# Optimization experiments

Measured on AMD Instinct MI355X. Metric: run time of the kernel, lower is better.

Reference implementation:

```python
import jax, jax.numpy as jnp
import numpy as np

N_NODES = 50000
N_EDGES = 800000
IN_DIM, HID_DIM, OUT_DIM = 128, 128, 64


def setup_inputs() -> dict:
    key = jax.random.key(0)
    ks = jax.random.split(key, 8)
    x = jax.random.normal(ks[0], (N_NODES, IN_DIM), dtype=jnp.float32)
    edge_index = jax.random.randint(ks[1], (2, N_EDGES), 0, N_NODES, dtype=jnp.int64)
    # GCNConv uses Glorot weights + zero bias; any random init is fine for a reference
    W1 = jax.random.normal(ks[2], (IN_DIM, HID_DIM), dtype=jnp.float32) / np.sqrt(IN_DIM)
    b1 = jnp.zeros((HID_DIM,), dtype=jnp.float32)
    W2 = jax.random.normal(ks[3], (HID_DIM, OUT_DIM), dtype=jnp.float32) / np.sqrt(HID_DIM)
    b2 = jnp.zeros((OUT_DIM,), dtype=jnp.float32)
    Wfc = jax.random.normal(ks[4], (OUT_DIM, 2), dtype=jnp.float32) / np.sqrt(OUT_DIM)
    bfc = jnp.zeros((2,), dtype=jnp.float32)
    return {"x": x, "edge_index": edge_index, "W1": W1, "b1": b1,
            "W2": W2, "b2": b2, "Wfc": Wfc, "bfc": bfc}


def _gcn_conv(x, src, dst, W, b, n_nodes):
    """PyG GCNConv: out = D^{-1/2} (A+I) D^{-1/2} (x W) + b."""
    xw = x @ W  # [N, F_out] transform before propagation
    ones = jnp.ones(src.shape[0], dtype=xw.dtype)
    deg = jax.ops.segment_sum(ones, dst, num_segments=n_nodes) + 1.0  # +1 for self-loop
    dinv = jax.lax.rsqrt(deg)
    norm = dinv[src] * dinv[dst]  # [E]
    msg = xw[src] * norm[:, None]  # gather + scale: [E, F_out]
    agg = jax.ops.segment_sum(msg, dst, num_segments=n_nodes)  # scatter-add
    agg = agg + xw * (dinv * dinv)[:, None]  # self-loop contribution (norm = 1/deg)
    return agg + b


def reference(x, edge_index, W1, b1, W2, b2, Wfc, bfc):
    n = x.shape[0]
    src, dst = edge_index[0], edge_index[1]
    h = jax.nn.relu(_gcn_conv(x, src, dst, W1, b1, n))
    # dropout is identity in eval mode
    h = _gcn_conv(h, src, dst, W2, b2, n)
    h = h @ Wfc + bfc
    return jax.nn.leaky_relu(h, negative_slope=0.01)
```

## Files before the change

### kernel.cpp

```cpp
#include <hip/hip_runtime.h>
#include <hip/hip_fp16.h>

#define IN_DIM 128
#define HID_DIM 128
#define OUT_DIM 64
#define BINW 128
#define BINSHIFT 7
#define MAXBIN 512
#define CAP 4096
#define CNTSTRIDE 16

__global__ __launch_bounds__(256) void k_scatter(const int* __restrict__ src,
                                                 const int* __restrict__ dst,
                                                 int* __restrict__ bin_cnt,
                                                 int* __restrict__ ovf_cnt,
                                                 unsigned int* __restrict__ ovf,
                                                 unsigned int* __restrict__ ebin,
                                                 int E, int nbin) {
    __shared__ int h[MAXBIN];
    __shared__ int base_s[MAXBIN];
    int t = threadIdx.x;
    for (int k = t; k < nbin; k += 256) h[k] = 0;
    __syncthreads();
    int per = E / gridDim.x;
    int ebeg = blockIdx.x * per;
    int eend = (blockIdx.x + 1 == gridDim.x) ? E : ebeg + per;
    for (int i = ebeg + t; i < eend; i += 256)
        atomicAdd(&h[dst[i] >> BINSHIFT], 1);
    __syncthreads();
    for (int k = t; k < nbin; k += 256) {
        int c = h[k];
        base_s[k] = (c > 0) ? atomicAdd(&bin_cnt[k * CNTSTRIDE], c) : 0;
        h[k] = 0;
    }
    __syncthreads();
    for (int i = ebeg + t; i < eend; i += 256) {
        unsigned int s = (unsigned int)src[i];
        unsigned int d = (unsigned int)dst[i];
        int b = (int)(d >> BINSHIFT);
        int pos = base_s[b] + atomicAdd(&h[b], 1);
        unsigned int packed = s | (d << 16);
        if (pos < CAP) ebin[(size_t)b * CAP + pos] = packed;
        else ovf[atomicAdd(ovf_cnt, 1)] = packed;
    }
}

__global__ __launch_bounds__(256) void k_fill(const unsigned int* __restrict__ ebin,
                                              const int* __restrict__ bin_cnt,
                                              const int* __restrict__ ovf_cnt,
                                              const unsigned int* __restrict__ ovf,
                                              int* __restrict__ row_ptr,
                                              unsigned short* __restrict__ degu,
                                              unsigned short* __restrict__ csr_src,
                                              float* __restrict__ dinv,
                                              const float* __restrict__ W2,
                                              const float* __restrict__ Wfc,
                                              const float* __restrict__ b2,
                                              const float* __restrict__ bfc,
                                              float* __restrict__ Wc,
                                              float* __restrict__ bc,
                                              int N, int nbin) {
    __shared__ int cnt[BINW];
    __shared__ int excl[BINW];
    __shared__ int start[BINW];
    int k = blockIdx.x;
    int node0 = k * BINW;
    int nn = min(BINW, N - node0);
    int t = threadIdx.x;
    if (t < BINW) cnt[t] = 0;
    __syncthreads();
    int cnt_k = min(bin_cnt[k * CNTSTRIDE], CAP);
    const unsigned int* seg = ebin + (size_t)k * CAP;
    for (int i = t; i < cnt_k; i += 256)
        atomicAdd(&cnt[(seg[i] >> 16) & (BINW - 1)], 1);
    int novf = *ovf_cnt;
    for (int i = t; i < novf; i += 256) {
        unsigned int e = ovf[i];
        if ((int)(e >> (16 + BINSHIFT)) == k)
            atomicAdd(&cnt[(e >> 16) & (BINW - 1)], 1);
    }
    __syncthreads();
    if (t < BINW) excl[t] = (t < nn) ? cnt[t] : 0;
    __syncthreads();
    for (int off = 1; off < BINW; off <<= 1) {
        int u = 0;
        if (t < BINW && t >= off) u = excl[t - off];
        __syncthreads();
        if (t < BINW) excl[t] += u;
        __syncthreads();
    }
    if (t < nn) {
        int deg = cnt[t];
        int e0 = k * CAP + excl[t] - deg;
        start[t] = e0;
        row_ptr[node0 + t] = e0;
        degu[node0 + t] = (unsigned short)deg;
        dinv[node0 + t] = rsqrtf((float)deg + 1.0f);
        cnt[t] = 0;
    }
    __syncthreads();
    for (int i = t; i < cnt_k; i += 256) {
        unsigned int e = seg[i];
        int dl = (e >> 16) & (BINW - 1);
        int slot = start[dl] + atomicAdd(&cnt[dl], 1);
        csr_src[slot] = (unsigned short)(e & 0xffffu);
    }
    for (int i = t; i < novf; i += 256) {
        unsigned int e = ovf[i];
        if ((int)(e >> (16 + BINSHIFT)) == k) {
            int dl = (e >> 16) & (BINW - 1);
            int slot = start[dl] + atomicAdd(&cnt[dl], 1);
            csr_src[slot] = (unsigned short)(e & 0xffffu);
        }
    }
    if (k == 0) {
        int kk = t >> 1, j = t & 1;
        float acc = 0.f;
#pragma unroll 8
        for (int m = 0; m < OUT_DIM; ++m) acc += W2[kk * OUT_DIM + m] * Wfc[m * 2 + j];
        Wc[kk * 2 + j] = acc;
        if (kk == 0) {
            float b = 0.f;
#pragma unroll 8
            for (int m = 0; m < OUT_DIM; ++m) b += b2[m] * Wfc[m * 2 + j];
            bc[j] = b + bfc[j];
        }
    }
}

__global__ __launch_bounds__(256) void k_gemm1(const float* __restrict__ x,
                                               const float* __restrict__ W,
                                               const float* __restrict__ dinv,
                                               __half* __restrict__ xwh, int N) {
    __shared__ float Ws[64][128];
    int tid = threadIdx.x;
    float4* Ws4 = (float4*)&Ws[0][0];
    int tx = tid & 15, ty = tid >> 4;
    int row0 = blockIdx.x * 128;
    int rows[8];
    const float* xr[8];
#pragma unroll
    for (int j = 0; j < 8; ++j) {
        int row = row0 + ty + 16 * j;
        rows[j] = row;
        if (row > N - 1) row = N - 1;
        xr[j] = x + (size_t)row * IN_DIM;
    }
    float4 aclo[8], achi[8];
#pragma unroll
    for (int j = 0; j < 8; ++j) {
        aclo[j] = make_float4(0.f, 0.f, 0.f, 0.f);
        achi[j] = make_float4(0.f, 0.f, 0.f, 0.f);
    }
#pragma unroll
    for (int ph = 0; ph < 2; ++ph) {
        const float4* W4 = (const float4*)(W + (size_t)ph * 64 * HID_DIM);
#pragma unroll
        for (int i = 0; i < 8; ++i) Ws4[tid + 256 * i] = W4[tid + 256 * i];
        __syncthreads();
#pragma unroll 2
        for (int k4 = 0; k4 < 16; ++k4) {
            float4 av[8];
#pragma unroll
            for (int j = 0; j < 8; ++j) av[j] = *(const float4*)(xr[j] + ph * 64 + k4 * 4);
#pragma unroll
            for (int kk = 0; kk < 4; ++kk) {
                float4 blo = *(const float4*)&Ws[k4 * 4 + kk][4 * tx];
                float4 bhi = *(const float4*)&Ws[k4 * 4 + kk][64 + 4 * tx];
#pragma unroll
                for (int j = 0; j < 8; ++j) {
                    float a = (kk == 0) ? av[j].x : (kk == 1) ? av[j].y : (kk == 2) ? av[j].z : av[j].w;
                    aclo[j].x += a * blo.x; aclo[j].y += a * blo.y;
                    aclo[j].z += a * blo.z; aclo[j].w += a * blo.w;
                    achi[j].x += a * bhi.x; achi[j].y += a * bhi.y;
                    achi[j].z += a * bhi.z; achi[j].w += a * bhi.w;
                }
            }
        }
        __syncthreads();
    }
#pragma unroll
    for (int j = 0; j < 8; ++j) {
        if (rows[j] < N) {
            float dd = dinv[rows[j]];
            union { __half2 h[2]; uint2 u; } lo, hi;
            lo.h[0] = __floats2half2_rn(aclo[j].x * dd, aclo[j].y * dd);
            lo.h[1] = __floats2half2_rn(aclo[j].z * dd, aclo[j].w * dd);
            hi.h[0] = __floats2half2_rn(achi[j].x * dd, achi[j].y * dd);
            hi.h[1] = __floats2half2_rn(achi[j].z * dd, achi[j].w * dd);
            uint2* p = (uint2*)(xwh + (size_t)rows[j] * HID_DIM);
            p[tx] = lo.u;
            p[16 + tx] = hi.u;
        }
    }
}

__global__ __launch_bounds__(256) void k_agg1z(const int* __restrict__ row_ptr,
                                               const unsigned short* __restrict__ degu,
                                               const unsigned short* __restrict__ csr_src,
                                               const float* __restrict__ dinv,
                                               const __half* __restrict__ xwh,
                                               const float* __restrict__ b1,
                                               const float* __restrict__ Wc,
                                               float* __restrict__ z, int N) {
    constexpr int F = HID_DIM;
    constexpr int L = F / 8;
    constexpr int EPW = 64 / L;
    __shared__ float Wcs[HID_DIM * 2];
    int tid = threadIdx.x;
    if (tid < 64) ((float4*)Wcs)[tid] = ((const float4*)Wc)[tid];
    __syncthreads();
    int node = (blockIdx.x * 256 + tid) >> 6;
    if (node >= N) return;
    int lane = tid & 63;
    int sub = lane / L;
    int c   = lane % L;
    int beg = row_ptr[node];
    int end = beg + degu[node];
    float dd = dinv[node];
    uint4 us = *(const uint4*)(xwh + (size_t)node * F + c * 8);
    float4 b1a = *(const float4*)(b1 + c * 8);
    float4 b1b = *(const float4*)(b1 + c * 8 + 4);
    float a0 = 0.f, a1 = 0.f, a2 = 0.f, a3 = 0.f;
    float a4 = 0.f, a5 = 0.f, a6 = 0.f, a7 = 0.f;
    auto acc = [&](uint4 u) {
        float2 v0 = __half22float2(*(__half2*)&u.x);
        float2 v1 = __half22float2(*(__half2*)&u.y);
        float2 v2 = __half22float2(*(__half2*)&u.z);
        float2 v3 = __half22float2(*(__half2*)&u.w);
        a0 += v0.x; a1 += v0.y; a2 += v1.x; a3 += v1.y;
        a4 += v2.x; a5 += v2.y; a6 += v3.x; a7 += v3.y;
    };
    int j = beg + sub;
    for (; j + 3 * EPW < end; j += 4 * EPW) {
        int s0 = csr_src[j];
        int s1 = csr_src[j + EPW];
        int s2 = csr_src[j + 2 * EPW];
        int s3 = csr_src[j + 3 * EPW];
        uint4 u0 = *(const uint4*)(xwh + (size_t)s0 * F + c * 8);
        uint4 u1 = *(const uint4*)(xwh + (size_t)s1 * F + c * 8);
        uint4 u2 = *(const uint4*)(xwh + (size_t)s2 * F + c * 8);
        uint4 u3 = *(const uint4*)(xwh + (size_t)s3 * F + c * 8);
        acc(u0); acc(u1); acc(u2); acc(u3);
    }
    for (; j < end; j += EPW) {
        int s = csr_src[j];
        acc(*(const uint4*)(xwh + (size_t)s * F + c * 8));
    }
#pragma unroll
    for (int off = L; off < 64; off <<= 1) {
        a0 += __shfl_xor(a0, off); a1 += __shfl_xor(a1, off);
        a2 += __shfl_xor(a2, off); a3 += __shfl_xor(a3, off);
        a4 += __shfl_xor(a4, off); a5 += __shfl_xor(a5, off);
        a6 += __shfl_xor(a6, off); a7 += __shfl_xor(a7, off);
    }
    float2 v0 = __half22float2(*(__half2*)&us.x);
    float2 v1 = __half22float2(*(__half2*)&us.y);
    float2 v2 = __half22float2(*(__half2*)&us.z);
    float2 v3 = __half22float2(*(__half2*)&us.w);
    float h[8];
    h[0] = fmaxf((a0 + v0.x) * dd + b1a.x, 0.f);
    h[1] = fmaxf((a1 + v0.y) * dd + b1a.y, 0.f);
    h[2] = fmaxf((a2 + v1.x) * dd + b1a.z, 0.f);
    h[3] = fmaxf((a3 + v1.y) * dd + b1a.w, 0.f);
    h[4] = fmaxf((a4 + v2.x) * dd + b1b.x, 0.f);
    h[5] = fmaxf((a5 + v2.y) * dd + b1b.y, 0.f);
    h[6] = fmaxf((a6 + v3.x) * dd + b1b.z, 0.f);
    h[7] = fmaxf((a7 + v3.y) * dd + b1b.w, 0.f);
    float o0 = 0.f, o1 = 0.f;
#pragma unroll
    for (int k = 0; k < 8; ++k) {
        o0 += h[k] * Wcs[(c * 8 + k) * 2 + 0];
        o1 += h[k] * Wcs[(c * 8 + k) * 2 + 1];
    }
#pragma unroll
    for (int off = 1; off < L; off <<= 1) {
        o0 += __shfl_xor(o0, off);
        o1 += __shfl_xor(o1, off);
    }
    if (lane == 0) {
        float2 r; r.x = o0 * dd; r.y = o1 * dd;
        *(float2*)(z + (size_t)node * 2) = r;
    }
}

__global__ __launch_bounds__(256) void k_agg2(const int* __restrict__ row_ptr,
                                              const unsigned short* __restrict__ degu,
                                              const unsigned short* __restrict__ csr_src,
                                              const float* __restrict__ dinv,
                                              const float* __restrict__ z,
                                              const float* __restrict__ bc,
                                              float* __restrict__ out, int N) {
    int tid = threadIdx.x;
    int gwave = (blockIdx.x * 256 + tid) >> 6;
    int lane = tid & 63;
    int grp = lane >> 3, li = lane & 7;
    int node = gwave * 8 + grp;
    if (node >= N) return;
    int beg = row_ptr[node];
    int end = beg + degu[node];
    float s0 = 0.f, s1 = 0.f;
    int j = beg + li;
    for (; j + 8 < end; j += 16) {
        int sa = csr_src[j];
        int sb = csr_src[j + 8];
        float2 za = *(const float2*)(z + (size_t)sa * 2);
        float2 zb = *(const float2*)(z + (size_t)sb * 2);
        s0 += za.x + zb.x; s1 += za.y + zb.y;
    }
    if (j < end) {
        int s = csr_src[j];
        float2 zv = *(const float2*)(z + (size_t)s * 2);
        s0 += zv.x; s1 += zv.y;
    }
#pragma unroll
    for (int off = 1; off < 8; off <<= 1) {
        s0 += __shfl_xor(s0, off);
        s1 += __shfl_xor(s1, off);
    }
    if (li == 0) {
        float2 zs = *(const float2*)(z + (size_t)node * 2);
        float dd = dinv[node];
        float o0 = (s0 + zs.x) * dd + bc[0];
        float o1 = (s1 + zs.y) * dd + bc[1];
        float2 r;
        r.x = o0 > 0.f ? o0 : 0.01f * o0;
        r.y = o1 > 0.f ? o1 : 0.01f * o1;
        *(float2*)(out + (size_t)node * 2) = r;
    }
}

extern "C" void kernel_launch(void* const* d_in, const int* in_sizes, int n_in,
                              void* d_out, int out_size, void* d_ws, size_t ws_size,
                              hipStream_t stream) {
    const float* x   = (const float*)d_in[0];
    const int*   ei  = (const int*)d_in[1];
    const float* W1  = (const float*)d_in[2];
    const float* b1  = (const float*)d_in[3];
    const float* W2  = (const float*)d_in[4];
    const float* b2  = (const float*)d_in[5];
    const float* Wfc = (const float*)d_in[6];
    const float* bfc = (const float*)d_in[7];

    const int N = in_sizes[0] / IN_DIM;
    const int E = in_sizes[1] / 2;
    const int* src = ei;
    const int* dst = ei + E;
    const int nbin = (N + BINW - 1) / BINW;

    char* base = (char*)d_ws;
    size_t off = 0;
    auto take = [&](size_t bytes) { size_t o = off; off = (off + bytes + 255) & ~(size_t)255; return (void*)(base + o); };
    int*    row_ptr  = (int*)take((size_t)N * 4);
    unsigned short* degu = (unsigned short*)take((size_t)N * 2);
    unsigned short* csr_src = (unsigned short*)take((size_t)nbin * CAP * 2);
    int*    bin_cnt  = (int*)take((size_t)(nbin * CNTSTRIDE + CNTSTRIDE) * 4);
    int*    ovf_cnt  = bin_cnt + nbin * CNTSTRIDE;
    unsigned int* ovf = (unsigned int*)take((size_t)E * 4);
    unsigned int* ebin = (unsigned int*)take((size_t)nbin * CAP * 4);
    float*  dinv     = (float*)take((size_t)N * 4);
    __half* xw1h     = (__half*)take((size_t)N * HID_DIM * 2);
    float*  zbuf     = (float*)take((size_t)N * 2 * 4);
    float*  Wc       = (float*)take((size_t)HID_DIM * 2 * 4);
    float*  bc       = (float*)take(2 * 4);

    hipMemsetAsync(bin_cnt, 0, (size_t)(nbin * CNTSTRIDE + CNTSTRIDE) * 4, stream);

    k_scatter<<<256, 256, 0, stream>>>(src, dst, bin_cnt, ovf_cnt, ovf, ebin, E, nbin);
    k_fill<<<nbin, 256, 0, stream>>>(ebin, bin_cnt, ovf_cnt, ovf, row_ptr, degu,
                                     csr_src, dinv, W2, Wfc, b2, bfc, Wc, bc, N, nbin);

    const int nTile = (N + 127) / 128;

    k_gemm1<<<nTile, 256, 0, stream>>>(x, W1, dinv, xw1h, N);
    k_agg1z<<<(N + 3) / 4, 256, 0, stream>>>(row_ptr, degu, csr_src, dinv, xw1h, b1, Wc, zbuf, N);
    const int nAgg2 = ((N + 7) / 8 * 64 + 255) / 256;
    k_agg2<<<nAgg2, 256, 0, stream>>>(row_ptr, degu, csr_src, dinv, zbuf, bc, (float*)d_out, N);
}
```

Before: 178.6 us.

## Fuse GEMM1 with edge binning scatter in one heterogeneous launch

Merges the edge-binning scatter kernel and the first dense transform into one launch, where the first blocks do the GEMM and the remaining blocks do the binning. This needs the GEMM to no longer depend on dinv, so the source-side normalization moves into the aggregation loop as a per-edge dinv[src] gather and FMA. Fewer launches and overlap of the compute-bound GEMM with the atomic-heavy scatter are the goal. The cost is an extra random 4-byte load per edge in k_agg1z, and the union shared memory sizes every block for the GEMM's 32 KB.

```diff
diff --git a/kernel.cpp b/kernel.cpp
--- a/kernel.cpp
+++ b/kernel.cpp
@@ -9,39 +9,111 @@
 #define MAXBIN 512
 #define CAP 4096
 #define CNTSTRIDE 16
-
-__global__ __launch_bounds__(256) void k_scatter(const int* __restrict__ src,
-                                                 const int* __restrict__ dst,
-                                                 int* __restrict__ bin_cnt,
-                                                 int* __restrict__ ovf_cnt,
-                                                 unsigned int* __restrict__ ovf,
-                                                 unsigned int* __restrict__ ebin,
-                                                 int E, int nbin) {
-    __shared__ int h[MAXBIN];
-    __shared__ int base_s[MAXBIN];
-    int t = threadIdx.x;
-    for (int k = t; k < nbin; k += 256) h[k] = 0;
-    __syncthreads();
-    int per = E / gridDim.x;
-    int ebeg = blockIdx.x * per;
-    int eend = (blockIdx.x + 1 == gridDim.x) ? E : ebeg + per;
-    for (int i = ebeg + t; i < eend; i += 256)
-        atomicAdd(&h[dst[i] >> BINSHIFT], 1);
-    __syncthreads();
-    for (int k = t; k < nbin; k += 256) {
-        int c = h[k];
-        base_s[k] = (c > 0) ? atomicAdd(&bin_cnt[k * CNTSTRIDE], c) : 0;
-        h[k] = 0;
-    }
-    __syncthreads();
-    for (int i = ebeg + t; i < eend; i += 256) {
-        unsigned int s = (unsigned int)src[i];
-        unsigned int d = (unsigned int)dst[i];
-        int b = (int)(d >> BINSHIFT);
-        int pos = base_s[b] + atomicAdd(&h[b], 1);
-        unsigned int packed = s | (d << 16);
-        if (pos < CAP) ebin[(size_t)b * CAP + pos] = packed;
-        else ovf[atomicAdd(ovf_cnt, 1)] = packed;
+#define SC_GRID 256
+
+__global__ __launch_bounds__(256) void k_build_gemm(const float* __restrict__ x,
+                                                    const float* __restrict__ W,
+                                                    __half* __restrict__ xwh,
+                                                    const int* __restrict__ src,
+                                                    const int* __restrict__ dst,
+                                                    int* __restrict__ bin_cnt,
+                                                    int* __restrict__ ovf_cnt,
+                                                    unsigned int* __restrict__ ovf,
+                                                    unsigned int* __restrict__ ebin,
+                                                    int N, int E, int nbin) {
+    __shared__ union SMem {
+        float Ws[64][128];
+        struct { int h[MAXBIN]; int base_s[MAXBIN]; } sc;
+    } smem;
+    const int nGemm = (N + 127) >> 7;
+    int tid = threadIdx.x;
+
+    if ((int)blockIdx.x < nGemm) {
+        float4* Ws4 = (float4*)&smem.Ws[0][0];
+        int tx = tid & 15, ty = tid >> 4;
+        int row0 = blockIdx.x * 128;
+        int rows[8];
+        const float* xr[8];
+#pragma unroll
+        for (int j = 0; j < 8; ++j) {
+            int row = row0 + ty + 16 * j;
+            rows[j] = row;
+            if (row > N - 1) row = N - 1;
+            xr[j] = x + (size_t)row * IN_DIM;
+        }
+        float4 aclo[8], achi[8];
+#pragma unroll
+        for (int j = 0; j < 8; ++j) {
+            aclo[j] = make_float4(0.f, 0.f, 0.f, 0.f);
+            achi[j] = make_float4(0.f, 0.f, 0.f, 0.f);
+        }
+#pragma unroll
+        for (int ph = 0; ph < 2; ++ph) {
+            const float4* W4 = (const float4*)(W + (size_t)ph * 64 * HID_DIM);
+#pragma unroll
+            for (int i = 0; i < 8; ++i) Ws4[tid + 256 * i] = W4[tid + 256 * i];
+            __syncthreads();
+#pragma unroll 2
+            for (int k4 = 0; k4 < 16; ++k4) {
+                float4 av[8];
+#pragma unroll
+                for (int j = 0; j < 8; ++j) av[j] = *(const float4*)(xr[j] + ph * 64 + k4 * 4);
+#pragma unroll
+                for (int kk = 0; kk < 4; ++kk) {
+                    float4 blo = *(const float4*)&smem.Ws[k4 * 4 + kk][4 * tx];
+                    float4 bhi = *(const float4*)&smem.Ws[k4 * 4 + kk][64 + 4 * tx];
+#pragma unroll
+                    for (int j = 0; j < 8; ++j) {
+                        float a = (kk == 0) ? av[j].x : (kk == 1) ? av[j].y : (kk == 2) ? av[j].z : av[j].w;
+                        aclo[j].x += a * blo.x; aclo[j].y += a * blo.y;
+                        aclo[j].z += a * blo.z; aclo[j].w += a * blo.w;
+                        achi[j].x += a * bhi.x; achi[j].y += a * bhi.y;
+                        achi[j].z += a * bhi.z; achi[j].w += a * bhi.w;
+                    }
+                }
+            }
+            __syncthreads();
+        }
+#pragma unroll
+        for (int j = 0; j < 8; ++j) {
+            if (rows[j] < N) {
+                union { __half2 h[2]; uint2 u; } lo, hi;
+                lo.h[0] = __floats2half2_rn(aclo[j].x, aclo[j].y);
+                lo.h[1] = __floats2half2_rn(aclo[j].z, aclo[j].w);
+                hi.h[0] = __floats2half2_rn(achi[j].x, achi[j].y);
+                hi.h[1] = __floats2half2_rn(achi[j].z, achi[j].w);
+                uint2* p = (uint2*)(xwh + (size_t)rows[j] * HID_DIM);
+                p[tx] = lo.u;
+                p[16 + tx] = hi.u;
+            }
+        }
+    } else {
+        int sb = blockIdx.x - nGemm;
+        int* h = smem.sc.h;
+        int* base_s = smem.sc.base_s;
+        for (int k = tid; k < nbin; k += 256) h[k] = 0;
+        __syncthreads();
+        int per = E / SC_GRID;
+        int ebeg = sb * per;
+        int eend = (sb + 1 == SC_GRID) ? E : ebeg + per;
+        for (int i = ebeg + tid; i < eend; i += 256)
+            atomicAdd(&h[dst[i] >> BINSHIFT], 1);
+        __syncthreads();
+        for (int k = tid; k < nbin; k += 256) {
+            int c = h[k];
+            base_s[k] = (c > 0) ? atomicAdd(&bin_cnt[k * CNTSTRIDE], c) : 0;
+            h[k] = 0;
+        }
+        __syncthreads();
+        for (int i = ebeg + tid; i < eend; i += 256) {
+            unsigned int s = (unsigned int)src[i];
+            unsigned int d = (unsigned int)dst[i];
+            int b = (int)(d >> BINSHIFT);
+            int pos = base_s[b] + atomicAdd(&h[b], 1);
+            unsigned int packed = s | (d << 16);
+            if (pos < CAP) ebin[(size_t)b * CAP + pos] = packed;
+            else ovf[atomicAdd(ovf_cnt, 1)] = packed;
+        }
     }
 }
 
@@ -128,73 +200,6 @@
     }
 }
 
-__global__ __launch_bounds__(256) void k_gemm1(const float* __restrict__ x,
-                                               const float* __restrict__ W,
-                                               const float* __restrict__ dinv,
-                                               __half* __restrict__ xwh, int N) {
-    __shared__ float Ws[64][128];
-    int tid = threadIdx.x;
-    float4* Ws4 = (float4*)&Ws[0][0];
-    int tx = tid & 15, ty = tid >> 4;
-    int row0 = blockIdx.x * 128;
-    int rows[8];
-    const float* xr[8];
-#pragma unroll
-    for (int j = 0; j < 8; ++j) {
-        int row = row0 + ty + 16 * j;
-        rows[j] = row;
-        if (row > N - 1) row = N - 1;
-        xr[j] = x + (size_t)row * IN_DIM;
-    }
-    float4 aclo[8], achi[8];
-#pragma unroll
-    for (int j = 0; j < 8; ++j) {
-        aclo[j] = make_float4(0.f, 0.f, 0.f, 0.f);
-        achi[j] = make_float4(0.f, 0.f, 0.f, 0.f);
-    }
-#pragma unroll
-    for (int ph = 0; ph < 2; ++ph) {
-        const float4* W4 = (const float4*)(W + (size_t)ph * 64 * HID_DIM);
-#pragma unroll
-        for (int i = 0; i < 8; ++i) Ws4[tid + 256 * i] = W4[tid + 256 * i];
-        __syncthreads();
-#pragma unroll 2
-        for (int k4 = 0; k4 < 16; ++k4) {
-            float4 av[8];
-#pragma unroll
-            for (int j = 0; j < 8; ++j) av[j] = *(const float4*)(xr[j] + ph * 64 + k4 * 4);
-#pragma unroll
-            for (int kk = 0; kk < 4; ++kk) {
-                float4 blo = *(const float4*)&Ws[k4 * 4 + kk][4 * tx];
-                float4 bhi = *(const float4*)&Ws[k4 * 4 + kk][64 + 4 * tx];
-#pragma unroll
-                for (int j = 0; j < 8; ++j) {
-                    float a = (kk == 0) ? av[j].x : (kk == 1) ? av[j].y : (kk == 2) ? av[j].z : av[j].w;
-                    aclo[j].x += a * blo.x; aclo[j].y += a * blo.y;
-                    aclo[j].z += a * blo.z; aclo[j].w += a * blo.w;
-                    achi[j].x += a * bhi.x; achi[j].y += a * bhi.y;
-                    achi[j].z += a * bhi.z; achi[j].w += a * bhi.w;
-                }
-            }
-        }
-        __syncthreads();
-    }
-#pragma unroll
-    for (int j = 0; j < 8; ++j) {
-        if (rows[j] < N) {
-            float dd = dinv[rows[j]];
-            union { __half2 h[2]; uint2 u; } lo, hi;
-            lo.h[0] = __floats2half2_rn(aclo[j].x * dd, aclo[j].y * dd);
-            lo.h[1] = __floats2half2_rn(aclo[j].z * dd, aclo[j].w * dd);
-            hi.h[0] = __floats2half2_rn(achi[j].x * dd, achi[j].y * dd);
-            hi.h[1] = __floats2half2_rn(achi[j].z * dd, achi[j].w * dd);
-            uint2* p = (uint2*)(xwh + (size_t)rows[j] * HID_DIM);
-            p[tx] = lo.u;
-            p[16 + tx] = hi.u;
-        }
-    }
-}
-
 __global__ __launch_bounds__(256) void k_agg1z(const int* __restrict__ row_ptr,
                                                const unsigned short* __restrict__ degu,
                                                const unsigned short* __restrict__ csr_src,
@@ -223,13 +228,15 @@
     float4 b1b = *(const float4*)(b1 + c * 8 + 4);
     float a0 = 0.f, a1 = 0.f, a2 = 0.f, a3 = 0.f;
     float a4 = 0.f, a5 = 0.f, a6 = 0.f, a7 = 0.f;
-    auto acc = [&](uint4 u) {
+    auto acc = [&](uint4 u, float w) {
         float2 v0 = __half22float2(*(__half2*)&u.x);
         float2 v1 = __half22float2(*(__half2*)&u.y);
         float2 v2 = __half22float2(*(__half2*)&u.z);
         float2 v3 = __half22float2(*(__half2*)&u.w);
-        a0 += v0.x; a1 += v0.y; a2 += v1.x; a3 += v1.y;
-        a4 += v2.x; a5 += v2.y; a6 += v3.x; a7 += v3.y;
+        a0 = fmaf(v0.x, w, a0); a1 = fmaf(v0.y, w, a1);
+        a2 = fmaf(v1.x, w, a2); a3 = fmaf(v1.y, w, a3);
+        a4 = fmaf(v2.x, w, a4); a5 = fmaf(v2.y, w, a5);
+        a6 = fmaf(v3.x, w, a6); a7 = fmaf(v3.y, w, a7);
     };
     int j = beg + sub;
     for (; j + 3 * EPW < end; j += 4 * EPW) {
@@ -241,11 +248,16 @@
         uint4 u1 = *(const uint4*)(xwh + (size_t)s1 * F + c * 8);
         uint4 u2 = *(const uint4*)(xwh + (size_t)s2 * F + c * 8);
         uint4 u3 = *(const uint4*)(xwh + (size_t)s3 * F + c * 8);
-        acc(u0); acc(u1); acc(u2); acc(u3);
+        float w0 = dinv[s0];
+        float w1 = dinv[s1];
+        float w2 = dinv[s2];
+        float w3 = dinv[s3];
+        acc(u0, w0); acc(u1, w1); acc(u2, w2); acc(u3, w3);
     }
     for (; j < end; j += EPW) {
         int s = csr_src[j];
-        acc(*(const uint4*)(xwh + (size_t)s * F + c * 8));
+        uint4 u = *(const uint4*)(xwh + (size_t)s * F + c * 8);
+        acc(u, dinv[s]);
     }
 #pragma unroll
     for (int off = L; off < 64; off <<= 1) {
@@ -259,14 +271,14 @@
     float2 v2 = __half22float2(*(__half2*)&us.z);
     float2 v3 = __half22float2(*(__half2*)&us.w);
     float h[8];
-    h[0] = fmaxf((a0 + v0.x) * dd + b1a.x, 0.f);
-    h[1] = fmaxf((a1 + v0.y) * dd + b1a.y, 0.f);
-    h[2] = fmaxf((a2 + v1.x) * dd + b1a.z, 0.f);
-    h[3] = fmaxf((a3 + v1.y) * dd + b1a.w, 0.f);
-    h[4] = fmaxf((a4 + v2.x) * dd + b1b.x, 0.f);
-    h[5] = fmaxf((a5 + v2.y) * dd + b1b.y, 0.f);
-    h[6] = fmaxf((a6 + v3.x) * dd + b1b.z, 0.f);
-    h[7] = fmaxf((a7 + v3.y) * dd + b1b.w, 0.f);
+    h[0] = fmaxf(fmaf(fmaf(v0.x, dd, a0), dd, b1a.x), 0.f);
+    h[1] = fmaxf(fmaf(fmaf(v0.y, dd, a1), dd, b1a.y), 0.f);
+    h[2] = fmaxf(fmaf(fmaf(v1.x, dd, a2), dd, b1a.z), 0.f);
+    h[3] = fmaxf(fmaf(fmaf(v1.y, dd, a3), dd, b1a.w), 0.f);
+    h[4] = fmaxf(fmaf(fmaf(v2.x, dd, a4), dd, b1b.x), 0.f);
+    h[5] = fmaxf(fmaf(fmaf(v2.y, dd, a5), dd, b1b.y), 0.f);
+    h[6] = fmaxf(fmaf(fmaf(v3.x, dd, a6), dd, b1b.z), 0.f);
+    h[7] = fmaxf(fmaf(fmaf(v3.y, dd, a7), dd, b1b.w), 0.f);
     float o0 = 0.f, o1 = 0.f;
 #pragma unroll
     for (int k = 0; k < 8; ++k) {
@@ -366,13 +378,11 @@
 
     hipMemsetAsync(bin_cnt, 0, (size_t)(nbin * CNTSTRIDE + CNTSTRIDE) * 4, stream);
 
-    k_scatter<<<256, 256, 0, stream>>>(src, dst, bin_cnt, ovf_cnt, ovf, ebin, E, nbin);
+    const int nGemm = (N + 127) / 128;
+    k_build_gemm<<<nGemm + SC_GRID, 256, 0, stream>>>(x, W1, xw1h, src, dst, bin_cnt,
+                                                      ovf_cnt, ovf, ebin, N, E, nbin);
     k_fill<<<nbin, 256, 0, stream>>>(ebin, bin_cnt, ovf_cnt, ovf, row_ptr, degu,
                                      csr_src, dinv, W2, Wfc, b2, bfc, Wc, bc, N, nbin);
-
-    const int nTile = (N + 127) / 128;
-
-    k_gemm1<<<nTile, 256, 0, stream>>>(x, W1, dinv, xw1h, N);
     k_agg1z<<<(N + 3) / 4, 256, 0, stream>>>(row_ptr, degu, csr_src, dinv, xw1h, b1, Wc, zbuf, N);
     const int nAgg2 = ((N + 7) / 8 * 64 + 255) / 256;
     k_agg2<<<nAgg2, 256, 0, stream>>>(row_ptr, degu, csr_src, dinv, zbuf, bc, (float*)d_out, N);
```

Measured after the change: 164.7 us. 1.08x faster.
